# Kernel tuning notes

Measured on AMD Instinct MI355X. Metric: run time of the kernel, lower is better.

The kernel has to match this reference:

```python
import jax, jax.numpy as jnp
import numpy as np

MAX_NUM_NODES = 100000
HIDDEN_DIM = 128
EVENT_SEQ_LEN = 262144


def setup_inputs() -> dict:
    key = jax.random.key(0)
    ks = jax.random.split(key, 12)
    L, H, N = EVENT_SEQ_LEN, HIDDEN_DIM, MAX_NUM_NODES
    return {
        "event_type_ids": jax.random.randint(ks[0], (L,), 0, 10),
        "src_ids": jax.random.randint(ks[1], (L,), 0, N),
        "src_mask": jax.random.uniform(ks[2], (L,), dtype=jnp.float32),
        "dst_ids": jax.random.randint(ks[3], (L,), 0, N),
        "dst_mask": jax.random.uniform(ks[4], (L,), dtype=jnp.float32),
        "event_embeddings": jax.random.normal(ks[5], (L, H), dtype=jnp.float32),
        "event_mask": jax.random.uniform(ks[6], (L,), dtype=jnp.float32),
        "event_timestamps": jax.random.uniform(ks[7], (L,), dtype=jnp.float32) * 100.0,
        # learned / state parameters
        "memory": jax.random.normal(ks[8], (N, H), dtype=jnp.float32),
        "last_update": jax.random.uniform(ks[9], (N,), dtype=jnp.float32) * 100.0,
        "time_w": jax.random.normal(ks[10], (H,), dtype=jnp.float32),
        "time_b": jax.random.normal(ks[11], (H,), dtype=jnp.float32),
    }


def _time_encode(t, w, b):
    # TGN time encoder: cos(Linear(1 -> H)(t))
    return jnp.cos(t[:, None] * w[None, :] + b[None, :])


def _scatter_mean(messages, ids, num_segments):
    sums = jax.ops.segment_sum(messages, ids, num_segments=num_segments)
    counts = jax.ops.segment_sum(jnp.ones((messages.shape[0],), messages.dtype), ids,
                                 num_segments=num_segments)
    return sums / jnp.maximum(counts, 1.0)[:, None]


def reference(event_type_ids, src_ids, src_mask, dst_ids, dst_mask,
              event_embeddings, event_mask, event_timestamps,
              memory, last_update, time_w, time_b):
    H = memory.shape[1]
    L = event_type_ids.shape[0]
    # message()
    event_type_embs = jnp.broadcast_to(
        event_type_ids.astype(memory.dtype)[:, None], (L, H))
    src_embs = memory[src_ids] * src_mask[:, None]
    dst_embs = memory[dst_ids] * dst_mask[:, None]
    src_last_update = last_update[src_ids]
    dst_last_update = last_update[dst_ids]
    # NOTE: original code multiplies src_last_update by dst_mask (faithful copy)
    src_timestamp_emb = _time_encode(event_timestamps - src_last_update * dst_mask, time_w, time_b)
    dst_timestamp_emb = _time_encode(event_timestamps - dst_last_update * dst_mask, time_w, time_b)
    src_messages = jnp.concatenate(
        [event_type_embs, src_embs, dst_embs, src_timestamp_emb, event_embeddings],
        axis=1) * event_mask[:, None]
    dst_messages = jnp.concatenate(
        [event_type_embs, dst_embs, src_embs, dst_timestamp_emb, event_embeddings],
        axis=1) * dst_mask[:, None]
    # agg_message(): scatter-mean over node ids
    src_agg = _scatter_mean(src_messages, src_ids, MAX_NUM_NODES)
    dst_agg = _scatter_mean(dst_messages, dst_ids, MAX_NUM_NODES)
    return jnp.stack([src_agg, dst_agg])  # (2, max_num_nodes, 5*hidden_dim)
```

## Files before the change

kernel.cpp:

```cpp
#include <hip/hip_runtime.h>

#define NODES 100000
#define HD 128
#define MSG 640
#define NS (2 * NODES)
#define CAP 24

typedef float f32x2 __attribute__((ext_vector_type(2)));
typedef float f32x4 __attribute__((ext_vector_type(4)));


__global__ void tgn_bucket_kernel(const int* __restrict__ event_type_ids,
                                  const int* __restrict__ src_ids,
                                  const float* __restrict__ src_mask,
                                  const int* __restrict__ dst_ids,
                                  const float* __restrict__ dst_mask,
                                  const float* __restrict__ event_mask,
                                  const float* __restrict__ event_timestamps,
                                  int* __restrict__ cnt,
                                  f32x4* __restrict__ rec, int L) {
    int i = blockIdx.x * blockDim.x + threadIdx.x;
    if (i >= L) return;
    int s = src_ids[i];
    int d = dst_ids[i];
    float sm = src_mask[i];
    float dm = dst_mask[i];
    float em = event_mask[i];
    float ts = event_timestamps[i];
    float typ = (float)event_type_ids[i];

    int ps = atomicAdd(&cnt[s], 1);
    if (ps < CAP) {
        size_t b = ((size_t)s * CAP + ps) * 2;
        rec[b]     = (f32x4){__int_as_float(d), __int_as_float(i), em, sm};
        rec[b + 1] = (f32x4){dm, dm, ts, typ};
    }

    int pd = atomicAdd(&cnt[NODES + d], 1);
    if (pd < CAP) {
        size_t b = ((size_t)(NODES + d) * CAP + pd) * 2;
        rec[b]     = (f32x4){__int_as_float(s), __int_as_float(i), dm, dm};
        rec[b + 1] = (f32x4){sm, dm, ts, typ};
    }
}

__global__ __launch_bounds__(256) void tgn_node_kernel(
        const float* __restrict__ event_embeddings,
        const float* __restrict__ memory,
        const float* __restrict__ last_update,
        const float* __restrict__ time_w,
        const float* __restrict__ time_b,
        const int* __restrict__ cnt,
        const f32x4* __restrict__ rec,
        float* __restrict__ out) {
    int wid = (int)((blockIdx.x * (long long)blockDim.x + threadIdx.x) >> 6);
    int lane = threadIdx.x & 63;
    if (wid >= NS) return;

    int node = (wid < NODES) ? wid : (wid - NODES);
    int c = __builtin_amdgcn_readfirstlane(cnt[wid]);
    int cc = (c < CAP) ? c : CAP;
    size_t base = (size_t)wid * (CAP * 2);

    const f32x2* mem2 = (const f32x2*)memory;
    const f32x2* emb2 = (const f32x2*)event_embeddings;
    f32x2 wv = ((const f32x2*)time_w)[lane];
    f32x2 bv = ((const f32x2*)time_b)[lane];
    f32x2 selfm = mem2[(size_t)node * 64 + lane];
    float lu = last_update[node];

    float a_typ = 0.f;
    f32x2 a_s = {0.f, 0.f};
    f32x2 a_o = {0.f, 0.f};
    f32x2 a_t = {0.f, 0.f};
    f32x2 a_e = {0.f, 0.f};

    for (int j = 0; j < cc; j += 2) {
        int has1 = (j + 1 < cc);
        int j1 = has1 ? j + 1 : j;
        f32x4 lo0 = rec[base + 2 * (size_t)j];
        f32x4 hi0 = rec[base + 2 * (size_t)j + 1];
        f32x4 lo1 = rec[base + 2 * (size_t)j1];
        f32x4 hi1 = rec[base + 2 * (size_t)j1 + 1];

        int other0 = __float_as_int(lo0.x), e0 = __float_as_int(lo0.y);
        int other1 = __float_as_int(lo1.x), e1 = __float_as_int(lo1.y);

        f32x2 mo0 = mem2[(size_t)other0 * 64 + lane];
        f32x2 ee0 = emb2[(size_t)e0 * 64 + lane];
        f32x2 mo1 = mem2[(size_t)other1 * 64 + lane];
        f32x2 ee1 = emb2[(size_t)e1 * 64 + lane];

        float scale0 = lo0.z,            selfk0 = lo0.w;
        float otherk0 = hi0.x, dm0 = hi0.y, ts0 = hi0.z, ty0 = hi0.w;
        float scale1 = has1 ? lo1.z : 0.f;
        float selfk1 = lo1.w;
        float otherk1 = hi1.x, dm1 = hi1.y, ts1 = hi1.z, ty1 = hi1.w;

        float tp0 = ts0 - lu * dm0;
        float tp1 = ts1 - lu * dm1;
        float t00 = __cosf(tp0 * wv.x + bv.x);
        float t01 = __cosf(tp0 * wv.y + bv.y);
        float t10 = __cosf(tp1 * wv.x + bv.x);
        float t11 = __cosf(tp1 * wv.y + bv.y);

        a_typ += ty0 * scale0 + ty1 * scale1;
        a_s.x += selfm.x * selfk0 * scale0 + selfm.x * selfk1 * scale1;
        a_s.y += selfm.y * selfk0 * scale0 + selfm.y * selfk1 * scale1;
        a_o.x += (mo0.x * otherk0) * scale0 + (mo1.x * otherk1) * scale1;
        a_o.y += (mo0.y * otherk0) * scale0 + (mo1.y * otherk1) * scale1;
        a_t.x += t00 * scale0 + t10 * scale1;
        a_t.y += t01 * scale0 + t11 * scale1;
        a_e.x += ee0.x * scale0 + ee1.x * scale1;
        a_e.y += ee0.y * scale0 + ee1.y * scale1;
    }

    float inv = (c > 0) ? (1.0f / (float)c) : 0.0f;
    f32x2* row = (f32x2*)(out + (size_t)wid * MSG);
    f32x2 v0 = {a_typ * inv, a_typ * inv};
    f32x2 v1 = {a_s.x * inv, a_s.y * inv};
    f32x2 v2 = {a_o.x * inv, a_o.y * inv};
    f32x2 v3 = {a_t.x * inv, a_t.y * inv};
    f32x2 v4 = {a_e.x * inv, a_e.y * inv};
    __builtin_nontemporal_store(v0, row + 0 * 64 + lane);
    __builtin_nontemporal_store(v1, row + 1 * 64 + lane);
    __builtin_nontemporal_store(v2, row + 2 * 64 + lane);
    __builtin_nontemporal_store(v3, row + 3 * 64 + lane);
    __builtin_nontemporal_store(v4, row + 4 * 64 + lane);
}

extern "C" void kernel_launch(void* const* d_in, const int* in_sizes, int n_in,
                              void* d_out, int out_size, void* d_ws, size_t ws_size,
                              hipStream_t stream) {
    const int* event_type_ids = (const int*)d_in[0];
    const int* src_ids = (const int*)d_in[1];
    const float* src_mask = (const float*)d_in[2];
    const int* dst_ids = (const int*)d_in[3];
    const float* dst_mask = (const float*)d_in[4];
    const float* event_embeddings = (const float*)d_in[5];
    const float* event_mask = (const float*)d_in[6];
    const float* event_timestamps = (const float*)d_in[7];
    const float* memory = (const float*)d_in[8];
    const float* last_update = (const float*)d_in[9];
    const float* time_w = (const float*)d_in[10];
    const float* time_b = (const float*)d_in[11];

    int L = in_sizes[0];
    float* out = (float*)d_out;

    int* cnt = (int*)d_ws;
    f32x4* rec = (f32x4*)((char*)d_ws + (size_t)NS * sizeof(int));

    (void)hipMemsetAsync(cnt, 0, (size_t)NS * sizeof(int), stream);

    int threads = 256;
    tgn_bucket_kernel<<<(L + threads - 1) / threads, threads, 0, stream>>>(
        event_type_ids, src_ids, src_mask, dst_ids, dst_mask,
        event_mask, event_timestamps, cnt, rec, L);

    long long total_threads = (long long)NS * 64;
    int blocks = (int)((total_threads + threads - 1) / threads);
    tgn_node_kernel<<<blocks, threads, 0, stream>>>(
        event_embeddings, memory, last_update, time_w, time_b,
        cnt, rec, out);
}
```

Measured before the change: 752.4 us.

## Process src and dst buckets per wave with half-wave split and f32x4 loads

Each 64-lane wave now handles one node's src and dst buckets. Each half-wave takes alternate events using 16-byte vector loads over the 128-wide rows, and the partial sums are merged with a cross-half shuffle. Each half then writes one of the two output rows. This halves the wave count and doubles per-lane load width so more events are in flight per wave, at the cost of more registers (two sets of accumulators) and shuffle reductions.

```diff
diff --git a/kernel.cpp b/kernel.cpp
--- a/kernel.cpp
+++ b/kernel.cpp
@@ -55,78 +55,108 @@
         float* __restrict__ out) {
     int wid = (int)((blockIdx.x * (long long)blockDim.x + threadIdx.x) >> 6);
     int lane = threadIdx.x & 63;
-    if (wid >= NS) return;
+    if (wid >= NODES) return;
+    int half = lane >> 5;
+    int sl = lane & 31;
 
-    int node = (wid < NODES) ? wid : (wid - NODES);
-    int c = __builtin_amdgcn_readfirstlane(cnt[wid]);
-    int cc = (c < CAP) ? c : CAP;
-    size_t base = (size_t)wid * (CAP * 2);
+    int node = wid;
+    int c0 = __builtin_amdgcn_readfirstlane(cnt[node]);
+    int c1 = __builtin_amdgcn_readfirstlane(cnt[NODES + node]);
+    int cc0 = (c0 < CAP) ? c0 : CAP;
+    int cc1 = (c1 < CAP) ? c1 : CAP;
 
-    const f32x2* mem2 = (const f32x2*)memory;
-    const f32x2* emb2 = (const f32x2*)event_embeddings;
-    f32x2 wv = ((const f32x2*)time_w)[lane];
-    f32x2 bv = ((const f32x2*)time_b)[lane];
-    f32x2 selfm = mem2[(size_t)node * 64 + lane];
+    const f32x4* mem4 = (const f32x4*)memory;
+    const f32x4* emb4 = (const f32x4*)event_embeddings;
+    f32x4 wv = ((const f32x4*)time_w)[sl];
+    f32x4 bv = ((const f32x4*)time_b)[sl];
+    f32x4 selfm = mem4[(size_t)node * 32 + sl];
     float lu = last_update[node];
 
-    float a_typ = 0.f;
-    f32x2 a_s = {0.f, 0.f};
-    f32x2 a_o = {0.f, 0.f};
-    f32x2 a_t = {0.f, 0.f};
-    f32x2 a_e = {0.f, 0.f};
+    float aty0 = 0.f; f32x4 as0 = {0,0,0,0}, ao0 = {0,0,0,0}, at0 = {0,0,0,0}, ae0 = {0,0,0,0};
+    float aty1 = 0.f; f32x4 as1 = {0,0,0,0}, ao1 = {0,0,0,0}, at1 = {0,0,0,0}, ae1 = {0,0,0,0};
 
-    for (int j = 0; j < cc; j += 2) {
-        int has1 = (j + 1 < cc);
-        int j1 = has1 ? j + 1 : j;
-        f32x4 lo0 = rec[base + 2 * (size_t)j];
-        f32x4 hi0 = rec[base + 2 * (size_t)j + 1];
-        f32x4 lo1 = rec[base + 2 * (size_t)j1];
-        f32x4 hi1 = rec[base + 2 * (size_t)j1 + 1];
-
-        int other0 = __float_as_int(lo0.x), e0 = __float_as_int(lo0.y);
-        int other1 = __float_as_int(lo1.x), e1 = __float_as_int(lo1.y);
-
-        f32x2 mo0 = mem2[(size_t)other0 * 64 + lane];
-        f32x2 ee0 = emb2[(size_t)e0 * 64 + lane];
-        f32x2 mo1 = mem2[(size_t)other1 * 64 + lane];
-        f32x2 ee1 = emb2[(size_t)e1 * 64 + lane];
-
-        float scale0 = lo0.z,            selfk0 = lo0.w;
-        float otherk0 = hi0.x, dm0 = hi0.y, ts0 = hi0.z, ty0 = hi0.w;
-        float scale1 = has1 ? lo1.z : 0.f;
-        float selfk1 = lo1.w;
-        float otherk1 = hi1.x, dm1 = hi1.y, ts1 = hi1.z, ty1 = hi1.w;
-
-        float tp0 = ts0 - lu * dm0;
-        float tp1 = ts1 - lu * dm1;
-        float t00 = __cosf(tp0 * wv.x + bv.x);
-        float t01 = __cosf(tp0 * wv.y + bv.y);
-        float t10 = __cosf(tp1 * wv.x + bv.x);
-        float t11 = __cosf(tp1 * wv.y + bv.y);
-
-        a_typ += ty0 * scale0 + ty1 * scale1;
-        a_s.x += selfm.x * selfk0 * scale0 + selfm.x * selfk1 * scale1;
-        a_s.y += selfm.y * selfk0 * scale0 + selfm.y * selfk1 * scale1;
-        a_o.x += (mo0.x * otherk0) * scale0 + (mo1.x * otherk1) * scale1;
-        a_o.y += (mo0.y * otherk0) * scale0 + (mo1.y * otherk1) * scale1;
-        a_t.x += t00 * scale0 + t10 * scale1;
-        a_t.y += t01 * scale0 + t11 * scale1;
-        a_e.x += ee0.x * scale0 + ee1.x * scale1;
-        a_e.y += ee0.y * scale0 + ee1.y * scale1;
+    {
+        size_t b = (size_t)node * (CAP * 2);
+        for (int j = 0; j < cc0; j += 2) {
+            int jj = j + half;
+            float valid = (jj < cc0) ? 1.f : 0.f;
+            int jc = (jj < cc0) ? jj : (cc0 - 1);
+            f32x4 lo = rec[b + 2 * (size_t)jc];
+            f32x4 hi = rec[b + 2 * (size_t)jc + 1];
+            int other = __float_as_int(lo.x);
+            int e     = __float_as_int(lo.y);
+            float scale = lo.z * valid;
+            float selfk = lo.w;
+            float otherk = hi.x, dm = hi.y, ts = hi.z, ty = hi.w;
+            f32x4 mo = mem4[(size_t)other * 32 + sl];
+            f32x4 ee = emb4[(size_t)e * 32 + sl];
+            float tp = ts - lu * dm;
+            f32x4 t;
+            t.x = __cosf(tp * wv.x + bv.x);
+            t.y = __cosf(tp * wv.y + bv.y);
+            t.z = __cosf(tp * wv.z + bv.z);
+            t.w = __cosf(tp * wv.w + bv.w);
+            aty0 += ty * scale;
+            as0 += selfm * (selfk * scale);
+            ao0 += mo * (otherk * scale);
+            at0 += t * scale;
+            ae0 += ee * scale;
+        }
+    }
+    {
+        size_t b = (size_t)(NODES + node) * (CAP * 2);
+        for (int j = 0; j < cc1; j += 2) {
+            int jj = j + half;
+            float valid = (jj < cc1) ? 1.f : 0.f;
+            int jc = (jj < cc1) ? jj : (cc1 - 1);
+            f32x4 lo = rec[b + 2 * (size_t)jc];
+            f32x4 hi = rec[b + 2 * (size_t)jc + 1];
+            int other = __float_as_int(lo.x);
+            int e     = __float_as_int(lo.y);
+            float scale = lo.z * valid;
+            float selfk = lo.w;
+            float otherk = hi.x, dm = hi.y, ts = hi.z, ty = hi.w;
+            f32x4 mo = mem4[(size_t)other * 32 + sl];
+            f32x4 ee = emb4[(size_t)e * 32 + sl];
+            float tp = ts - lu * dm;
+            f32x4 t;
+            t.x = __cosf(tp * wv.x + bv.x);
+            t.y = __cosf(tp * wv.y + bv.y);
+            t.z = __cosf(tp * wv.z + bv.z);
+            t.w = __cosf(tp * wv.w + bv.w);
+            aty1 += ty * scale;
+            as1 += selfm * (selfk * scale);
+            ao1 += mo * (otherk * scale);
+            at1 += t * scale;
+            ae1 += ee * scale;
+        }
     }
 
-    float inv = (c > 0) ? (1.0f / (float)c) : 0.0f;
-    f32x2* row = (f32x2*)(out + (size_t)wid * MSG);
-    f32x2 v0 = {a_typ * inv, a_typ * inv};
-    f32x2 v1 = {a_s.x * inv, a_s.y * inv};
-    f32x2 v2 = {a_o.x * inv, a_o.y * inv};
-    f32x2 v3 = {a_t.x * inv, a_t.y * inv};
-    f32x2 v4 = {a_e.x * inv, a_e.y * inv};
-    __builtin_nontemporal_store(v0, row + 0 * 64 + lane);
-    __builtin_nontemporal_store(v1, row + 1 * 64 + lane);
-    __builtin_nontemporal_store(v2, row + 2 * 64 + lane);
-    __builtin_nontemporal_store(v3, row + 3 * 64 + lane);
-    __builtin_nontemporal_store(v4, row + 4 * 64 + lane);
+    #define XS(v) ((v) + __shfl_xor((v), 32))
+    #define XV(v) { v.x = XS(v.x); v.y = XS(v.y); v.z = XS(v.z); v.w = XS(v.w); }
+    aty0 = XS(aty0); aty1 = XS(aty1);
+    XV(as0); XV(ao0); XV(at0); XV(ae0);
+    XV(as1); XV(ao1); XV(at1); XV(ae1);
+    #undef XV
+    #undef XS
+
+    float inv0 = (c0 > 0) ? (1.0f / (float)c0) : 0.0f;
+    float inv1 = (c1 > 0) ? (1.0f / (float)c1) : 0.0f;
+
+    float invh = half ? inv1 : inv0;
+    float tyv = (half ? aty1 : aty0) * invh;
+    f32x4 vty = {tyv, tyv, tyv, tyv};
+    f32x4 vs = (half ? as1 : as0) * invh;
+    f32x4 vo = (half ? ao1 : ao0) * invh;
+    f32x4 vt = (half ? at1 : at0) * invh;
+    f32x4 ve = (half ? ae1 : ae0) * invh;
+
+    f32x4* o4 = (f32x4*)(out + (size_t)(half ? (NODES + node) : node) * MSG);
+    __builtin_nontemporal_store(vty, o4 + 0 * 32 + sl);
+    __builtin_nontemporal_store(vs,  o4 + 1 * 32 + sl);
+    __builtin_nontemporal_store(vo,  o4 + 2 * 32 + sl);
+    __builtin_nontemporal_store(vt,  o4 + 3 * 32 + sl);
+    __builtin_nontemporal_store(ve,  o4 + 4 * 32 + sl);
 }
 
 extern "C" void kernel_launch(void* const* d_in, const int* in_sizes, int n_in,
@@ -158,7 +188,7 @@
         event_type_ids, src_ids, src_mask, dst_ids, dst_mask,
         event_mask, event_timestamps, cnt, rec, L);
 
-    long long total_threads = (long long)NS * 64;
+    long long total_threads = (long long)NODES * 64;
     int blocks = (int)((total_threads + threads - 1) / threads);
     tgn_node_kernel<<<blocks, threads, 0, stream>>>(
         event_embeddings, memory, last_update, time_w, time_b,
```

Result: no change. 741.2 us (-1.5%).
